# Performance work log

Hardware: AMD Instinct MI355X
Metric: run time of the kernel (lower is better)

## Reference

```python
import jax, jax.numpy as jnp
import numpy as np

D = 1024
H = 16
HD = D // H
T = 2048
B = 2
EPS = 1e-6


def rmsnorm(x, w):
    xf = x.astype(jnp.float32)
    n = xf * jax.lax.rsqrt(jnp.mean(xf * xf, axis=-1, keepdims=True) + EPS)
    return n.astype(x.dtype) * w


def setup_inputs() -> dict:
    key = jax.random.key(0)
    ks = jax.random.split(key, 12)
    s_in = 1.0 / np.sqrt(D)
    s_h = 1.0 / np.sqrt(HD * H)
    s_ff = 1.0 / np.sqrt(4 * D)
    return {
        "x": jax.random.normal(ks[0], (B, T, D), jnp.float32),
        "wq": jax.random.normal(ks[1], (H, D, HD), jnp.float32) * s_in,
        "wk": jax.random.normal(ks[2], (H, D, HD), jnp.float32) * s_in,
        "wv": jax.random.normal(ks[3], (H, D, HD), jnp.float32) * s_in,
        "w_proj": jax.random.normal(ks[4], (D, D), jnp.float32) * s_h,
        "b_proj": jax.random.normal(ks[5], (D,), jnp.float32) * 0.01,
        "w1": jax.random.normal(ks[6], (D, 8 * D), jnp.float32) * s_in,
        "b1": jax.random.normal(ks[7], (8 * D,), jnp.float32) * 0.01,
        "w2": jax.random.normal(ks[8], (4 * D, D), jnp.float32) * s_ff,
        "b2": jax.random.normal(ks[9], (D,), jnp.float32) * 0.01,
        "g1": jnp.ones((D,), jnp.float32),
        "g2": jnp.ones((D,), jnp.float32),
    }


def reference(x, wq, wk, wv, w_proj, b_proj, w1, b1, w2, b2, g1, g2):
    # --- attention sub-block ---
    xn = rmsnorm(x, g1)
    q = jnp.einsum("btd,hde->bhte", xn, wq)  # [B,H,T,HD]
    k = jnp.einsum("btd,hde->bhte", xn, wk)
    v = jnp.einsum("btd,hde->bhte", xn, wv)
    scores = jnp.einsum("bhte,bhse->bhts", q, k) * (HD ** -0.5)
    causal = jnp.tril(jnp.ones((T, T), bool))
    scores = jnp.where(causal, scores, -jnp.inf)
    attn = jax.nn.softmax(scores, axis=-1)
    o = jnp.einsum("bhts,bhse->bhte", attn, v)  # [B,H,T,HD]
    o = o.transpose(0, 2, 1, 3).reshape(B, T, H * HD)  # concat heads
    x = x + o @ w_proj + b_proj
    # --- GLU FFN sub-block ---
    xn2 = rmsnorm(x, g2)
    h = xn2 @ w1 + b1  # [B,T,8D]
    a, b = jnp.split(h, 2, axis=-1)
    glu = a * jax.nn.sigmoid(b)  # [B,T,4D]
    x = x + glu @ w2 + b2
    return x
```

## Files before the change

### kernel.cpp

```cpp
#include <hip/hip_runtime.h>


typedef __attribute__((ext_vector_type(4))) float f32x4;
typedef __attribute__((ext_vector_type(8))) short short8;

typedef __attribute__((address_space(1))) const void gvoid;
typedef __attribute__((address_space(3))) void lvoid;

static __device__ __forceinline__ void gl_lds16(const void* g, void* l) {
  __builtin_amdgcn_global_load_lds((gvoid*)g, (lvoid*)l, 16, 0, 0);
}

static __device__ __forceinline__ unsigned short f2bf(float f) {
  union { float f; unsigned u; } v; v.f = f;
  unsigned r = v.u + 0x7fffu + ((v.u >> 16) & 1u);
  return (unsigned short)(r >> 16);
}
static __device__ __forceinline__ float to_f32(float v) { return v; }
static __device__ __forceinline__ float to_f32(unsigned short v) {
  union { unsigned u; float f; } x; x.u = ((unsigned)v) << 16; return x.f;
}

static __device__ __forceinline__ f32x4 mfma16(short8 a, short8 b, f32x4 c) {
  return __builtin_amdgcn_mfma_f32_16x16x32_bf16(a, b, c, 0, 0, 0);
}

template <typename Tin>
__global__ __launch_bounds__(256) void transpose_cvt(
    const Tin* __restrict__ in, unsigned short* __restrict__ out,
    int in_ld, long in_bstride, int out_ld, long out_bstride)
{
  __shared__ float tile[64][65];
  const Tin* inp = in + (long)blockIdx.z * in_bstride;
  unsigned short* outp = out + (long)blockIdx.z * out_bstride;
  int r0 = blockIdx.y * 64, c0 = blockIdx.x * 64;
  int tx = threadIdx.x & 63, ty = threadIdx.x >> 6;
#pragma unroll
  for (int i = ty; i < 64; i += 4)
    tile[i][tx] = to_f32(inp[(long)(r0 + i) * in_ld + (c0 + tx)]);
  __syncthreads();
#pragma unroll
  for (int i = ty; i < 64; i += 4)
    outp[(long)(c0 + i) * out_ld + (r0 + tx)] = f2bf(tile[tx][i]);
}

__global__ __launch_bounds__(256) void rmsnorm_k(
    const float* __restrict__ x, const float* __restrict__ g,
    unsigned short* __restrict__ out)
{
  int row = blockIdx.x;
  int t = threadIdx.x;
  float4 v = ((const float4*)(x + (long)row * 1024))[t];
  float ss = v.x * v.x + v.y * v.y + v.z * v.z + v.w * v.w;
#pragma unroll
  for (int ofs = 32; ofs; ofs >>= 1) ss += __shfl_down(ss, ofs);
  __shared__ float red[4];
  if ((t & 63) == 0) red[t >> 6] = ss;
  __syncthreads();
  float sc = rsqrtf((red[0] + red[1] + red[2] + red[3]) * (1.0f / 1024.0f) + 1e-6f);
  float4 gv = ((const float4*)g)[t];
  ushort4 o4;
  o4.x = f2bf(v.x * sc * gv.x); o4.y = f2bf(v.y * sc * gv.y);
  o4.z = f2bf(v.z * sc * gv.z); o4.w = f2bf(v.w * sc * gv.w);
  ((ushort4*)(out + (long)row * 1024))[t] = o4;
}

template <int EPI, int BM, int WM_, int WN_, bool GLUB>
__global__ __launch_bounds__(256, 2) void gemm_bt(
    const unsigned short* __restrict__ A, const unsigned short* __restrict__ Bt,
    unsigned short* __restrict__ outb, float* __restrict__ outf,
    const float* __restrict__ res, const float* __restrict__ bias,
    int K, int lda, int ldbt, int ldout)
{
  constexpr int FM = BM / (16 * WM_);
  constexpr int FN = 128 / (16 * WN_);
  constexpr int AR = BM / 32;
  __shared__ alignas(16) unsigned short Asm_[BM * 64];
  __shared__ alignas(16) unsigned short Bsm_[128 * 64];
  const int tid = threadIdx.x, lane = tid & 63, wave = tid >> 6;
  const int lr = lane & 15, lg = lane >> 4;
  const int wr = wave / WN_, wc = wave % WN_;
  const int m0 = blockIdx.y * BM;

  f32x4 acc[FM][FN];
#pragma unroll
  for (int mi = 0; mi < FM; mi++)
#pragma unroll
    for (int ni = 0; ni < FN; ni++) acc[mi][ni] = f32x4{0.f, 0.f, 0.f, 0.f};

  int br_[4], bu_[4];
  long brow[4];
#pragma unroll
  for (int i = 0; i < 4; i++) {
    int U = tid + 256 * i;
    br_[i] = U >> 3;
    bu_[i] = ((U & 7) ^ (br_[i] & 7)) * 8;
    if (GLUB)
      brow[i] = (br_[i] < 64) ? (long)(blockIdx.x * 64 + br_[i])
                              : (long)(4096 + blockIdx.x * 64 + br_[i] - 64);
    else
      brow[i] = (long)blockIdx.x * 128 + br_[i];
  }
  int ar_[AR], au_[AR];
#pragma unroll
  for (int i = 0; i < AR; i++) {
    int U = tid + 256 * i;
    ar_[i] = U >> 3;
    au_[i] = ((U & 7) ^ (ar_[i] & 7)) * 8;
  }

  for (int k0 = 0; k0 < K; k0 += 64) {
#pragma unroll
    for (int i = 0; i < 4; i++)
      gl_lds16(Bt + brow[i] * ldbt + k0 + bu_[i],
               (char*)Bsm_ + (wave * 64 + 256 * i) * 16);
#pragma unroll
    for (int i = 0; i < AR; i++)
      gl_lds16(A + (long)(m0 + ar_[i]) * lda + k0 + au_[i],
               (char*)Asm_ + (wave * 64 + 256 * i) * 16);
    __syncthreads();

    short8 af[FM][2], bfr[FN][2];
#pragma unroll
    for (int mi = 0; mi < FM; mi++) {
      int row = wr * 16 * FM + mi * 16 + lr;
#pragma unroll
      for (int kk = 0; kk < 2; kk++) {
        int off = row * 128 + (((kk * 4 + lg) ^ (row & 7)) & 7) * 16;
        af[mi][kk] = *(const short8*)((const char*)Asm_ + off);
      }
    }
#pragma unroll
    for (int ni = 0; ni < FN; ni++) {
      int row = wc * 16 * FN + ni * 16 + lr;
#pragma unroll
      for (int kk = 0; kk < 2; kk++) {
        int off = row * 128 + (((kk * 4 + lg) ^ (row & 7)) & 7) * 16;
        bfr[ni][kk] = *(const short8*)((const char*)Bsm_ + off);
      }
    }
    __builtin_amdgcn_s_setprio(1);
#pragma unroll
    for (int kk = 0; kk < 2; kk++)
#pragma unroll
      for (int mi = 0; mi < FM; mi++)
#pragma unroll
        for (int ni = 0; ni < FN; ni++)
          acc[mi][ni] = mfma16(af[mi][kk], bfr[ni][kk], acc[mi][ni]);
    __builtin_amdgcn_s_setprio(0);
    __syncthreads();
  }

  const int rb = m0 + wr * 16 * FM + 4 * lg;
  if constexpr (EPI == 0) {
#pragma unroll
    for (int mi = 0; mi < FM; mi++)
#pragma unroll
      for (int ni = 0; ni < FN; ni++) {
        int col = blockIdx.x * 128 + wc * 16 * FN + ni * 16 + lr;
#pragma unroll
        for (int r = 0; r < 4; r++)
          outb[(long)(rb + mi * 16 + r) * ldout + col] = f2bf(acc[mi][ni][r]);
      }
  } else if constexpr (EPI == 1) {
#pragma unroll
    for (int mi = 0; mi < FM; mi++)
#pragma unroll
      for (int ni = 0; ni < FN; ni++) {
        int col = blockIdx.x * 128 + wc * 16 * FN + ni * 16 + lr;
        float bv = bias[col];
#pragma unroll
        for (int r = 0; r < 4; r++) {
          long idx = (long)(rb + mi * 16 + r) * ldout + col;
          outf[idx] = acc[mi][ni][r] + res[idx] + bv;
        }
      }
  } else {
#pragma unroll
    for (int mi = 0; mi < FM; mi++)
#pragma unroll
      for (int ni = 0; ni < FN / 2; ni++) {
        int col = blockIdx.x * 64 + ni * 16 + lr;
        float ba = bias[col], bb2 = bias[4096 + col];
#pragma unroll
        for (int r = 0; r < 4; r++) {
          float a = acc[mi][ni][r] + ba;
          float b = acc[mi][ni + FN / 2][r] + bb2;
          float s = 1.0f / (1.0f + __expf(-b));
          outb[(long)(rb + mi * 16 + r) * ldout + col] = f2bf(a * s);
        }
      }
  }
}

__global__ __launch_bounds__(256, 2) void attn_k(
    const unsigned short* __restrict__ qkv, const unsigned short* __restrict__ vt,
    unsigned short* __restrict__ o)
{
  __shared__ alignas(16) unsigned short Ksm[2 * 128 * 64];
  __shared__ alignas(16) unsigned short Vsm[2 * 64 * 128];
  __shared__ alignas(16) unsigned short Psm[4][16 * 128];
  const int tid = threadIdx.x, lane = tid & 63, wave = tid >> 6;
  const int lr = lane & 15, lg = lane >> 4;
  const int bh = blockIdx.y, b = bh >> 4, h = bh & 15;
  const int ia = blockIdx.x;
  const int tA0 = ia * 64, tB0 = (31 - ia) * 64;
  const int nchA = (ia + 2) >> 1, nchB = (33 - ia) >> 1;
  const float NEGINF = -__builtin_inff();

  short8 qfA[2], qfB[2];
  {
    const unsigned short* qp =
        qkv + (long)(b * 2048 + tA0 + wave * 16 + lr) * 3072 + h * 64 + lg * 8;
    qfA[0] = *(const short8*)qp;  qfA[1] = *(const short8*)(qp + 32);
    qp = qkv + (long)(b * 2048 + tB0 + wave * 16 + lr) * 3072 + h * 64 + lg * 8;
    qfB[0] = *(const short8*)qp;  qfB[1] = *(const short8*)(qp + 32);
  }
  f32x4 oA[4], oB[4];
#pragma unroll
  for (int n = 0; n < 4; n++) { oA[n] = f32x4{0,0,0,0}; oB[n] = f32x4{0,0,0,0}; }
  float mA = NEGINF, lA = 0.f, mB = NEGINF, lB = 0.f;

  const long kbase = (long)(b * 2048) * 3072 + 1024 + h * 64;
  const long vbase = (long)bh * 64 * 2048;

  auto stage = [&](int buf, int c) {
    const int s0 = c * 128;
#pragma unroll
    for (int i = 0; i < 4; i++) {
      int U = tid + 256 * i;
      int kr = U >> 3, ku = (U ^ kr) & 7;
      gl_lds16(qkv + kbase + (long)(s0 + kr) * 3072 + ku * 8,
               (char*)Ksm + (buf * 1024 + wave * 64 + 256 * i) * 16);
      int vr = U >> 4, vu = (U & 8) | ((U ^ vr) & 7);
      gl_lds16(vt + vbase + (long)vr * 2048 + s0 + vu * 8,
               (char*)Vsm + (buf * 1024 + wave * 64 + 256 * i) * 16);
    }
  };

  char* pb = (char*)&Psm[wave][0];

  auto process = [&](const short8* qf, f32x4* o_acc, float& m, float& l,
                     const char* kb, const char* vb, int s0, int qg, bool diag) {
    f32x4 s[8];
#pragma unroll
    for (int n = 0; n < 8; n++) s[n] = f32x4{0.f, 0.f, 0.f, 0.f};
    __builtin_amdgcn_s_setprio(1);
#pragma unroll
    for (int n = 0; n < 8; n++) {
      int row = n * 16 + lr;
#pragma unroll
      for (int kk = 0; kk < 2; kk++) {
        int off = row * 128 + (((kk * 4 + lg) ^ row) & 7) * 16;
        short8 kf = *(const short8*)(kb + off);
        s[n] = mfma16(kf, qf[kk], s[n]);
      }
    }
    __builtin_amdgcn_s_setprio(0);
#pragma unroll
    for (int n = 0; n < 8; n++)
#pragma unroll
      for (int r = 0; r < 4; r++) {
        float v = s[n][r] * 0.125f;
        if (diag && (s0 + n * 16 + 4 * lg + r > qg)) v = NEGINF;
        s[n][r] = v;
      }
    float t[8];
#pragma unroll
    for (int n = 0; n < 8; n++)
      t[n] = fmaxf(fmaxf(s[n][0], s[n][1]), fmaxf(s[n][2], s[n][3]));
    float mx = fmaxf(fmaxf(fmaxf(t[0], t[1]), fmaxf(t[2], t[3])),
                     fmaxf(fmaxf(t[4], t[5]), fmaxf(t[6], t[7])));
    mx = fmaxf(mx, __shfl_xor(mx, 16));
    mx = fmaxf(mx, __shfl_xor(mx, 32));
    if (!__all(mx <= m + 8.0f)) {
      float mn = fmaxf(m, mx);
      float alpha = __expf(m - mn);
      m = mn;
      l *= alpha;
#pragma unroll
      for (int r = 0; r < 4; r++) {
        float ar = __shfl(alpha, 4 * lg + r);
#pragma unroll
        for (int n = 0; n < 4; n++) o_acc[n][r] *= ar;
      }
    }
    float sum = 0.f;
#pragma unroll
    for (int n = 0; n < 8; n++)
#pragma unroll
      for (int r = 0; r < 4; r++) {
        float p = __expf(s[n][r] - m);
        s[n][r] = p;
        sum += p;
      }
    sum += __shfl_xor(sum, 16);
    sum += __shfl_xor(sum, 32);
    l += sum;
#pragma unroll
    for (int n = 0; n < 8; n++) {
      unsigned lo = (unsigned)f2bf(s[n][0]) | ((unsigned)f2bf(s[n][1]) << 16);
      unsigned hi = (unsigned)f2bf(s[n][2]) | ((unsigned)f2bf(s[n][3]) << 16);
      int u = 2 * n + (lg >> 1);
      int su = (u & 8) | ((u ^ lr) & 7);
      *(uint2*)(pb + lr * 256 + su * 16 + 8 * (lg & 1)) = uint2{lo, hi};
    }
    asm volatile("s_waitcnt lgkmcnt(0)" ::: "memory");
    __builtin_amdgcn_sched_barrier(0);
    short8 pa[4];
#pragma unroll
    for (int ks = 0; ks < 4; ks++) {
      int u = 4 * ks + lg;
      int su = (u & 8) | ((u ^ lr) & 7);
      pa[ks] = *(const short8*)(pb + lr * 256 + su * 16);
    }
    __builtin_amdgcn_s_setprio(1);
#pragma unroll
    for (int n = 0; n < 4; n++) {
      int row = n * 16 + lr;
#pragma unroll
      for (int ks = 0; ks < 4; ks++) {
        int u = 4 * ks + lg;
        int su = (u & 8) | ((u ^ row) & 7);
        short8 vf = *(const short8*)(vb + row * 256 + su * 16);
        o_acc[n] = mfma16(pa[ks], vf, o_acc[n]);
      }
    }
    __builtin_amdgcn_s_setprio(0);
  };

  stage(0, 0);
  __syncthreads();

  const int qgA = tA0 + wave * 16 + lr, qgB = tB0 + wave * 16 + lr;
  for (int c = 0; c < nchB; c++) {
    if (c + 1 < nchB) stage((c + 1) & 1, c + 1);
    const char* kb = (const char*)Ksm + (c & 1) * 16384;
    const char* vb = (const char*)Vsm + (c & 1) * 16384;
    const int s0 = c * 128;
    if (c < nchA) process(qfA, oA, mA, lA, kb, vb, s0, qgA, c == nchA - 1);
    process(qfB, oB, mB, lB, kb, vb, s0, qgB, c == nchB - 1);
    __syncthreads();
  }

  auto finish = [&](const f32x4* o_acc, float l, int t0) {
#pragma unroll
    for (int r = 0; r < 4; r++) {
      float inv = 1.0f / __shfl(l, 4 * lg + r);
      int trow = t0 + wave * 16 + 4 * lg + r;
#pragma unroll
      for (int n = 0; n < 4; n++)
        o[(long)(b * 2048 + trow) * 1024 + h * 64 + n * 16 + lr] =
            f2bf(o_acc[n][r] * inv);
    }
  };
  finish(oA, lA, tA0);
  finish(oB, lB, tB0);
}

extern "C" void kernel_launch(void* const* d_in, const int* in_sizes, int n_in,
                              void* d_out, int out_size, void* d_ws, size_t ws_size,
                              hipStream_t stream) {
  const float* x     = (const float*)d_in[0];
  const float* wq    = (const float*)d_in[1];
  const float* wk    = (const float*)d_in[2];
  const float* wv    = (const float*)d_in[3];
  const float* wproj = (const float*)d_in[4];
  const float* bproj = (const float*)d_in[5];
  const float* w1    = (const float*)d_in[6];
  const float* b1    = (const float*)d_in[7];
  const float* w2    = (const float*)d_in[8];
  const float* b2    = (const float*)d_in[9];
  const float* g1    = (const float*)d_in[10];
  const float* g2    = (const float*)d_in[11];
  (void)in_sizes; (void)n_in; (void)out_size; (void)ws_size;

  char* ws = (char*)d_ws;
  unsigned short* wt_qkv = (unsigned short*)(ws);
  unsigned short* wpt    = (unsigned short*)(ws + (6ul << 20));
  unsigned short* w1t    = (unsigned short*)(ws + (8ul << 20));
  unsigned short* w2t    = (unsigned short*)(ws + (24ul << 20));
  unsigned short* xn     = (unsigned short*)(ws + (32ul << 20));
  unsigned short* qkv    = (unsigned short*)(ws + (40ul << 20));
  unsigned short* vt     = (unsigned short*)(ws + (64ul << 20));
  unsigned short* glu    = (unsigned short*)(ws + (40ul << 20));
  unsigned short* obuf   = (unsigned short*)(ws + (72ul << 20));
  float*          x1     = (float*)(ws + (80ul << 20));
  float* outf = (float*)d_out;

  transpose_cvt<float><<<dim3(1, 16, 16), 256, 0, stream>>>(
      wq, wt_qkv, 64, (long)1024 * 64, 1024, (long)64 * 1024);
  transpose_cvt<float><<<dim3(1, 16, 16), 256, 0, stream>>>(
      wk, wt_qkv + 1024ul * 1024, 64, (long)1024 * 64, 1024, (long)64 * 1024);
  transpose_cvt<float><<<dim3(1, 16, 16), 256, 0, stream>>>(
      wv, wt_qkv + 2048ul * 1024, 64, (long)1024 * 64, 1024, (long)64 * 1024);
  transpose_cvt<float><<<dim3(16, 16, 1), 256, 0, stream>>>(
      wproj, wpt, 1024, 0, 1024, 0);
  transpose_cvt<float><<<dim3(128, 16, 1), 256, 0, stream>>>(
      w1, w1t, 8192, 0, 1024, 0);
  transpose_cvt<float><<<dim3(16, 64, 1), 256, 0, stream>>>(
      w2, w2t, 1024, 0, 4096, 0);

  rmsnorm_k<<<4096, 256, 0, stream>>>(x, g1, xn);

  gemm_bt<0, 128, 2, 2, false><<<dim3(24, 32), 256, 0, stream>>>(
      xn, wt_qkv, qkv, nullptr, nullptr, nullptr, 1024, 1024, 1024, 3072);

  transpose_cvt<unsigned short><<<dim3(1, 32, 16), 256, 0, stream>>>(
      qkv + 2048, vt, 3072, 64, 2048, (long)64 * 2048);
  transpose_cvt<unsigned short><<<dim3(1, 32, 16), 256, 0, stream>>>(
      qkv + 2048ul * 3072 + 2048, vt + 16ul * 64 * 2048, 3072, 64, 2048, (long)64 * 2048);

  attn_k<<<dim3(16, 32), 256, 0, stream>>>(qkv, vt, obuf);

  gemm_bt<1, 64, 2, 2, false><<<dim3(8, 64), 256, 0, stream>>>(
      obuf, wpt, nullptr, x1, x, bproj, 1024, 1024, 1024, 1024);

  rmsnorm_k<<<4096, 256, 0, stream>>>(x1, g2, xn);

  gemm_bt<2, 128, 4, 1, true><<<dim3(64, 32), 256, 0, stream>>>(
      xn, w1t, glu, nullptr, nullptr, b1, 1024, 1024, 1024, 4096);

  gemm_bt<1, 64, 2, 2, false><<<dim3(8, 64), 256, 0, stream>>>(
      glu, w2t, nullptr, outf, x1, b2, 4096, 4096, 4096, 1024);
}
```

Measured before the change: 304.5 us.

## Merge QKV weight transposes into one launch and interleave GEMM tile loads

Replaces the three separate transpose launches for wq, wk and wv with a single repack kernel that selects its source by grid z, cutting two kernel launches. In the GEMM main loop the A and B global-to-LDS loads are interleaved in one loop that shares row and swizzle index registers. The s_setprio calls around the MFMA block are also removed, which may change how waves are scheduled against each other.

```diff
diff --git a/kernel.cpp b/kernel.cpp
--- a/kernel.cpp
+++ b/kernel.cpp
@@ -42,6 +42,25 @@
 #pragma unroll
   for (int i = ty; i < 64; i += 4)
     outp[(long)(c0 + i) * out_ld + (r0 + tx)] = f2bf(tile[tx][i]);
+}
+
+__global__ __launch_bounds__(256) void qkvw_repack(
+    const float* __restrict__ wq, const float* __restrict__ wk,
+    const float* __restrict__ wv, unsigned short* __restrict__ out)
+{
+  __shared__ float tile[64][65];
+  const int z = blockIdx.z, head = z & 15, src = z >> 4;
+  const float* inp = (src == 0 ? wq : src == 1 ? wk : wv) + (long)head * 1024 * 64;
+  unsigned short* outp = out + ((long)src * 1024 + head * 64) * 1024;
+  int r0 = blockIdx.y * 64;
+  int tx = threadIdx.x & 63, ty = threadIdx.x >> 6;
+#pragma unroll
+  for (int i = ty; i < 64; i += 4)
+    tile[i][tx] = inp[(long)(r0 + i) * 64 + tx];
+  __syncthreads();
+#pragma unroll
+  for (int i = ty; i < 64; i += 4)
+    outp[(long)i * 1024 + r0 + tx] = f2bf(tile[tx][i]);
 }
 
 __global__ __launch_bounds__(256) void rmsnorm_k(
@@ -88,36 +107,29 @@
 #pragma unroll
     for (int ni = 0; ni < FN; ni++) acc[mi][ni] = f32x4{0.f, 0.f, 0.f, 0.f};
 
-  int br_[4], bu_[4];
+  int rr_[4], ru_[4];
   long brow[4];
 #pragma unroll
   for (int i = 0; i < 4; i++) {
     int U = tid + 256 * i;
-    br_[i] = U >> 3;
-    bu_[i] = ((U & 7) ^ (br_[i] & 7)) * 8;
+    rr_[i] = U >> 3;
+    ru_[i] = ((U & 7) ^ (rr_[i] & 7)) * 8;
     if (GLUB)
-      brow[i] = (br_[i] < 64) ? (long)(blockIdx.x * 64 + br_[i])
-                              : (long)(4096 + blockIdx.x * 64 + br_[i] - 64);
+      brow[i] = (rr_[i] < 64) ? (long)(blockIdx.x * 64 + rr_[i])
+                              : (long)(4096 + blockIdx.x * 64 + rr_[i] - 64);
     else
-      brow[i] = (long)blockIdx.x * 128 + br_[i];
+      brow[i] = (long)blockIdx.x * 128 + rr_[i];
   }
-  int ar_[AR], au_[AR];
-#pragma unroll
-  for (int i = 0; i < AR; i++) {
-    int U = tid + 256 * i;
-    ar_[i] = U >> 3;
-    au_[i] = ((U & 7) ^ (ar_[i] & 7)) * 8;
-  }
 
   for (int k0 = 0; k0 < K; k0 += 64) {
 #pragma unroll
-    for (int i = 0; i < 4; i++)
-      gl_lds16(Bt + brow[i] * ldbt + k0 + bu_[i],
+    for (int i = 0; i < 4; i++) {
+      if (i < AR)
+        gl_lds16(A + (long)(m0 + rr_[i]) * lda + k0 + ru_[i],
+                 (char*)Asm_ + (wave * 64 + 256 * i) * 16);
+      gl_lds16(Bt + brow[i] * ldbt + k0 + ru_[i],
                (char*)Bsm_ + (wave * 64 + 256 * i) * 16);
-#pragma unroll
-    for (int i = 0; i < AR; i++)
-      gl_lds16(A + (long)(m0 + ar_[i]) * lda + k0 + au_[i],
-               (char*)Asm_ + (wave * 64 + 256 * i) * 16);
+    }
     __syncthreads();
 
     short8 af[FM][2], bfr[FN][2];
@@ -139,7 +151,6 @@
         bfr[ni][kk] = *(const short8*)((const char*)Bsm_ + off);
       }
     }
-    __builtin_amdgcn_s_setprio(1);
 #pragma unroll
     for (int kk = 0; kk < 2; kk++)
 #pragma unroll
@@ -147,7 +158,6 @@
 #pragma unroll
         for (int ni = 0; ni < FN; ni++)
           acc[mi][ni] = mfma16(af[mi][kk], bfr[ni][kk], acc[mi][ni]);
-    __builtin_amdgcn_s_setprio(0);
     __syncthreads();
   }
 
@@ -388,12 +398,7 @@
   float*          x1     = (float*)(ws + (80ul << 20));
   float* outf = (float*)d_out;
 
-  transpose_cvt<float><<<dim3(1, 16, 16), 256, 0, stream>>>(
-      wq, wt_qkv, 64, (long)1024 * 64, 1024, (long)64 * 1024);
-  transpose_cvt<float><<<dim3(1, 16, 16), 256, 0, stream>>>(
-      wk, wt_qkv + 1024ul * 1024, 64, (long)1024 * 64, 1024, (long)64 * 1024);
-  transpose_cvt<float><<<dim3(1, 16, 16), 256, 0, stream>>>(
-      wv, wt_qkv + 2048ul * 1024, 64, (long)1024 * 64, 1024, (long)64 * 1024);
+  qkvw_repack<<<dim3(1, 16, 48), 256, 0, stream>>>(wq, wk, wv, wt_qkv);
   transpose_cvt<float><<<dim3(16, 16, 1), 256, 0, stream>>>(
       wproj, wpt, 1024, 0, 1024, 0);
   transpose_cvt<float><<<dim3(128, 16, 1), 256, 0, stream>>>(
```

After: 293.5 us. 3.6% less time.
